# Optimization experiments

Measured on AMD Instinct MI355X. Metric: run time of the kernel, lower is better.

Reference implementation:

```python
import jax, jax.numpy as jnp
import numpy as np

EPS = 1e-5  # BatchNorm1d default eps
N1, N2 = 4096, 4096


def _encoder(x, W1, b1, W2, b2, W3, b3, gamma, beta):
    # fc1: Linear(node_num,256)+ReLU; fc2: Linear(256,128)+ReLU; fc3: Linear(128,64)+BN(train-mode)+ReLU
    h = jax.nn.relu(x @ W1.T + b1)
    h = jax.nn.relu(h @ W2.T + b2)
    h = h @ W3.T + b3
    m = h.mean(axis=0)
    v = ((h - m) ** 2).mean(axis=0)  # biased variance, as BN training mode
    return jax.nn.relu((h - m) / jnp.sqrt(v + EPS) * gamma + beta)


def _self_attention(x, adj, alpha):
    # vectorized form of the per-node double loop:
    # tmp_i = (sum_{j: adj[i,j]==1} alpha[i,j] * x[j]) / degree_i + x[i]  if degree_i != 0 else 0
    mask = (adj == 1.0).astype(x.dtype)           # [N,N]
    deg = adj.sum(axis=1, keepdims=True)          # [N,1]
    agg = (mask * alpha) @ x                      # [N,64] masked SpMM
    return jnp.where(deg != 0, agg / deg + x, jnp.zeros((), x.dtype))


def setup_inputs() -> dict:
    key = jax.random.key(0)
    ks = jax.random.split(key, 20)
    d = {}
    d["x1"] = jax.random.normal(ks[0], (N1, N1), jnp.float32)
    d["x2"] = jax.random.normal(ks[1], (N2, N2), jnp.float32)
    d["adj1"] = jax.random.bernoulli(ks[2], 0.01, (N1, N1)).astype(jnp.float32)
    d["adj2"] = jax.random.bernoulli(ks[3], 0.01, (N2, N2)).astype(jnp.float32)
    def lin(k, fan_out, fan_in):
        bound = 1.0 / np.sqrt(fan_in)
        k1, k2 = jax.random.split(k)
        return (jax.random.uniform(k1, (fan_out, fan_in), jnp.float32, -bound, bound),
                jax.random.uniform(k2, (fan_out,), jnp.float32, -bound, bound))
    d["e1_W1"], d["e1_b1"] = lin(ks[4], 256, N1)
    d["e1_W2"], d["e1_b2"] = lin(ks[5], 128, 256)
    d["e1_W3"], d["e1_b3"] = lin(ks[6], 64, 128)
    d["e1_gamma"] = jnp.ones((64,), jnp.float32)
    d["e1_beta"] = jnp.zeros((64,), jnp.float32)
    d["e2_W1"], d["e2_b1"] = lin(ks[7], 256, N2)
    d["e2_W2"], d["e2_b2"] = lin(ks[8], 128, 256)
    d["e2_W3"], d["e2_b3"] = lin(ks[9], 64, 128)
    d["e2_gamma"] = jnp.ones((64,), jnp.float32)
    d["e2_beta"] = jnp.zeros((64,), jnp.float32)
    d["alpha1"] = jax.random.uniform(ks[10], (N1, N1), jnp.float32)
    d["alpha2"] = jax.random.uniform(ks[11], (N2, N2), jnp.float32)
    d["Wc"], d["bc"] = lin(ks[12], 2, (N1 + N2) * 64)
    return d


def reference(x1, x2, adj1, adj2,
              e1_W1, e1_b1, e1_W2, e1_b2, e1_W3, e1_b3, e1_gamma, e1_beta,
              e2_W1, e2_b1, e2_W2, e2_b2, e2_W3, e2_b3, e2_gamma, e2_beta,
              alpha1, alpha2, Wc, bc):
    h1 = _encoder(x1, e1_W1, e1_b1, e1_W2, e1_b2, e1_W3, e1_b3, e1_gamma, e1_beta)
    h2 = _encoder(x2, e2_W1, e2_b1, e2_W2, e2_b2, e2_W3, e2_b3, e2_gamma, e2_beta)
    h1 = _self_attention(h1, adj1, alpha1)
    h2 = _self_attention(h2, adj2, alpha2)
    feat = jnp.concatenate([h1, h2], axis=0).reshape(1, -1)  # [1,(N1+N2)*64]
    return feat @ Wc.T + bc  # [1,2] logits (softmax is defined but unused in forward)
```

## Files before the change

kernel.cpp:

```cpp
#include <hip/hip_runtime.h>
#include <cstddef>
#include <cstdint>


#define NN 4096
#define HDIM 64
#define ENC_OUT (NN * HDIM)

typedef _Float16 half8 __attribute__((ext_vector_type(8)));
typedef _Float16 half4 __attribute__((ext_vector_type(4)));
typedef float v4f __attribute__((ext_vector_type(4)));

__device__ __forceinline__ void gld_lds16(const void* g, void* l) {
    __builtin_amdgcn_global_load_lds(
        (const __attribute__((address_space(1))) void*)g,
        (__attribute__((address_space(3))) void*)l, 16, 0, 0);
}

struct GemmP {
    const void*     A[2];
    const _Float16* B[2];
    const float*    bias[2];
    void*           C[2];
};

template<int NI, bool A16, int OUT, bool RELU>
__global__ __launch_bounds__(256) void gemm_kernel(GemmP p, int M, int lda, int Ksub)
{
    constexpr int N = NI * 64;
    __shared__ char Bs[NI * 4 * 1024];

    const int tid = threadIdx.x;
    const int wave = tid >> 6, lane = tid & 63;
    const int l16 = lane & 15, quad = lane >> 4;
    const int enc = blockIdx.z, split = blockIdx.x;
    const int m0 = blockIdx.y * 32;
    const int kOff = split * Ksub;
    const int nsteps = Ksub >> 5;

    const _Float16* __restrict__ Bp = p.B[enc];
    const char* Abase = (const char*)p.A[enc];

    const size_t aoff0 = (size_t)(m0 + l16) * lda + kOff + quad * 8;
    const size_t aoff1 = aoff0 + (size_t)16 * lda;

    half8 na0, na1;
    float4 nf0lo, nf0hi, nf1lo, nf1hi;
    auto loadA = [&](int s) {
        if constexpr (A16) {
            const _Float16* A = (const _Float16*)Abase;
            na0 = *(const half8*)(A + aoff0 + s * 32);
            na1 = *(const half8*)(A + aoff1 + s * 32);
        } else {
            const float* A = (const float*)Abase;
            nf0lo = *(const float4*)(A + aoff0 + s * 32);
            nf0hi = *(const float4*)(A + aoff0 + s * 32 + 4);
            nf1lo = *(const float4*)(A + aoff1 + s * 32);
            nf1hi = *(const float4*)(A + aoff1 + s * 32 + 4);
        }
    };

    v4f acc[2][NI];
#pragma unroll
    for (int mi = 0; mi < 2; mi++)
#pragma unroll
        for (int ni = 0; ni < NI; ni++) acc[mi][ni] = (v4f){0.f, 0.f, 0.f, 0.f};

    loadA(0);

    for (int s = 0; s < nsteps; ++s) {
#pragma unroll
        for (int ni = 0; ni < NI; ni++) {
            const int T = wave * NI + ni;
            const _Float16* g = Bp + (size_t)(T * 16 + l16) * lda + kOff + s * 32 + quad * 8;
            gld_lds16(g, &Bs[T * 1024]);
        }
        half8 ca0, ca1;
        if constexpr (A16) {
            ca0 = na0; ca1 = na1;
        } else {
            ca0[0] = (_Float16)nf0lo.x; ca0[1] = (_Float16)nf0lo.y;
            ca0[2] = (_Float16)nf0lo.z; ca0[3] = (_Float16)nf0lo.w;
            ca0[4] = (_Float16)nf0hi.x; ca0[5] = (_Float16)nf0hi.y;
            ca0[6] = (_Float16)nf0hi.z; ca0[7] = (_Float16)nf0hi.w;
            ca1[0] = (_Float16)nf1lo.x; ca1[1] = (_Float16)nf1lo.y;
            ca1[2] = (_Float16)nf1lo.z; ca1[3] = (_Float16)nf1lo.w;
            ca1[4] = (_Float16)nf1hi.x; ca1[5] = (_Float16)nf1hi.y;
            ca1[6] = (_Float16)nf1hi.z; ca1[7] = (_Float16)nf1hi.w;
        }
        if (s + 1 < nsteps) loadA(s + 1);

        __builtin_amdgcn_s_waitcnt(0x0F70);

#pragma unroll
        for (int ni = 0; ni < NI; ni++) {
            half8 bf = *(const half8*)&Bs[(wave * NI + ni) * 1024 + lane * 16];
            acc[0][ni] = __builtin_amdgcn_mfma_f32_16x16x32_f16(ca0, bf, acc[0][ni], 0, 0, 0);
            acc[1][ni] = __builtin_amdgcn_mfma_f32_16x16x32_f16(ca1, bf, acc[1][ni], 0, 0, 0);
        }
    }

#pragma unroll
    for (int mi = 0; mi < 2; mi++)
#pragma unroll
        for (int ni = 0; ni < NI; ni++) {
            const int col = wave * NI * 16 + ni * 16 + l16;
#pragma unroll
            for (int i = 0; i < 4; i++) {
                const int row = m0 + mi * 16 + quad * 4 + i;
                float v = acc[mi][ni][i];
                if constexpr (OUT == 2) {
                    ((_Float16*)p.C[0])[((size_t)(split * 2 + enc) * M + row) * N + col]
                        = (_Float16)v;
                } else {
                    v += p.bias[enc][col];
                    if (RELU) v = fmaxf(v, 0.f);
                    if constexpr (OUT == 0)
                        ((_Float16*)p.C[enc])[(size_t)row * N + col] = (_Float16)v;
                    else
                        ((float*)p.C[enc])[(size_t)row * N + col] = v;
                }
            }
        }
}

__global__ __launch_bounds__(256) void fc1_reduce_kernel(const _Float16* __restrict__ part,
                                                         const float* __restrict__ b0,
                                                         const float* __restrict__ b1,
                                                         _Float16* __restrict__ h1h)
{
    const size_t i = ((size_t)blockIdx.x * 256 + threadIdx.x) * 8;
    const int e = (int)(i >> 20);
    const size_t r = i & ((1u << 20) - 1);
    half8 p0 = *(const half8*)&part[((size_t)(0 * 2 + e) << 20) + r];
    half8 p1 = *(const half8*)&part[((size_t)(1 * 2 + e) << 20) + r];
    const int col = (int)(i & 255);
    const float* bs = e ? b1 : b0;
    float4 ba = *(const float4*)&bs[col];
    float4 bb = *(const float4*)&bs[col + 4];
    float b[8] = {ba.x, ba.y, ba.z, ba.w, bb.x, bb.y, bb.z, bb.w};
    half8 o;
#pragma unroll
    for (int j = 0; j < 8; j++) {
        float v = (float)p0[j] + (float)p1[j] + b[j];
        o[j] = (_Float16)fmaxf(v, 0.f);
    }
    *(half8*)&h1h[i] = o;
}

struct CvtJob { const float* s; _Float16* d; int n4; };
struct CvtP { CvtJob j[6]; };

__global__ __launch_bounds__(256) void cvt_all_kernel(CvtP p)
{
    int i = blockIdx.x * 256 + threadIdx.x;
#pragma unroll
    for (int k = 0; k < 6; k++) {
        if (i < p.j[k].n4) {
            float4 v = ((const float4*)p.j[k].s)[i];
            half4 h;
            h[0] = (_Float16)v.x; h[1] = (_Float16)v.y;
            h[2] = (_Float16)v.z; h[3] = (_Float16)v.w;
            ((half4*)p.j[k].d)[i] = h;
            return;
        }
        i -= p.j[k].n4;
    }
}

__global__ __launch_bounds__(256) void bn_stat1_kernel(const float* __restrict__ h3,
                                                       float* __restrict__ bnp)
{
    const int enc = blockIdx.y, b = blockIdx.x;
    const int c = threadIdx.x & 63, rg = threadIdx.x >> 6;
    const float* h = h3 + (size_t)enc * ENC_OUT + (size_t)b * 128 * HDIM;
    float s = 0.f, q = 0.f;
    for (int r = rg; r < 128; r += 4) {
        float v = h[(size_t)r * HDIM + c];
        s += v; q += v * v;
    }
    __shared__ float ss[4][64], sq[4][64];
    ss[rg][c] = s; sq[rg][c] = q;
    __syncthreads();
    if (threadIdx.x < 64) {
        float S = ss[0][c] + ss[1][c] + ss[2][c] + ss[3][c];
        float Q = sq[0][c] + sq[1][c] + sq[2][c] + sq[3][c];
        bnp[(size_t)(enc * 32 + b) * 128 + c] = S;
        bnp[(size_t)(enc * 32 + b) * 128 + 64 + c] = Q;
    }
}

__global__ void bn_stat2_kernel(const float* __restrict__ bnp, float* __restrict__ stats)
{
    const int enc = blockIdx.x, c = threadIdx.x;
    float s = 0.f, q = 0.f;
    for (int b = 0; b < 32; b++) {
        s += bnp[(size_t)(enc * 32 + b) * 128 + c];
        q += bnp[(size_t)(enc * 32 + b) * 128 + 64 + c];
    }
    float mean = s * (1.f / NN);
    float var = q * (1.f / NN) - mean * mean;
    stats[enc * 128 + c] = mean;
    stats[enc * 128 + 64 + c] = rsqrtf(var + 1e-5f);
}

__global__ __launch_bounds__(256) void bn_apply_kernel(const float* __restrict__ h3,
                                                       const float* __restrict__ stats,
                                                       const float* __restrict__ g0,
                                                       const float* __restrict__ g1,
                                                       const float* __restrict__ be0,
                                                       const float* __restrict__ be1,
                                                       float* __restrict__ hn)
{
    const int idx = blockIdx.x * 256 + threadIdx.x;
    const int enc = idx >> 18;
    const int c = idx & 63;
    const float* g = enc ? g1 : g0;
    const float* be = enc ? be1 : be0;
    const float m = stats[enc * 128 + c];
    const float rs = stats[enc * 128 + 64 + c];
    float v = (h3[idx] - m) * rs * g[c] + be[c];
    hn[idx] = fmaxf(v, 0.f);
}

__global__ __launch_bounds__(256) void att_kernel(const float* __restrict__ adj1,
                                                  const float* __restrict__ adj2,
                                                  const float* __restrict__ al1,
                                                  const float* __restrict__ al2,
                                                  const float* __restrict__ hn,
                                                  float* __restrict__ out)
{
    const int enc = blockIdx.y;
    const float* adj = enc ? adj2 : adj1;
    const float* al = enc ? al2 : al1;
    const float* h = hn + (size_t)enc * ENC_OUT;
    float* o = out + (size_t)enc * ENC_OUT;
    const int i = blockIdx.x;
    const int tid = threadIdx.x;

    __shared__ int s_cnt;
    __shared__ int s_j[128];
    __shared__ float s_w[128];
    __shared__ float s_acc[4][64];

    if (tid == 0) s_cnt = 0;
    __syncthreads();

    const float* arow = adj + (size_t)i * NN;
    const int jb = tid * 16;
#pragma unroll
    for (int q = 0; q < 4; q++) {
        float4 a = *(const float4*)&arow[jb + q * 4];
        if (a.x == 1.f) { int p = atomicAdd(&s_cnt, 1); if (p < 128) s_j[p] = jb + q * 4 + 0; }
        if (a.y == 1.f) { int p = atomicAdd(&s_cnt, 1); if (p < 128) s_j[p] = jb + q * 4 + 1; }
        if (a.z == 1.f) { int p = atomicAdd(&s_cnt, 1); if (p < 128) s_j[p] = jb + q * 4 + 2; }
        if (a.w == 1.f) { int p = atomicAdd(&s_cnt, 1); if (p < 128) s_j[p] = jb + q * 4 + 3; }
    }
    __syncthreads();
    const int cnt = min(s_cnt, 128);

    const float* alrow = al + (size_t)i * NN;
    for (int t = tid; t < cnt; t += 256) s_w[t] = alrow[s_j[t]];
    __syncthreads();

    const int c = tid & 63;
    const int g = tid >> 6;
    float acc = 0.f;
    for (int t = g; t < cnt; t += 4) acc += s_w[t] * h[(size_t)s_j[t] * HDIM + c];
    s_acc[g][c] = acc;
    __syncthreads();

    if (tid < 64) {
        float r;
        if (cnt != 0) {
            r = (s_acc[0][c] + s_acc[1][c] + s_acc[2][c] + s_acc[3][c]) / (float)cnt
                + h[(size_t)i * HDIM + c];
        } else {
            r = 0.f;
        }
        o[(size_t)i * HDIM + c] = r;
    }
}

#define FDIM (2 * ENC_OUT)

__global__ __launch_bounds__(256) void final_partial_kernel(const float* __restrict__ feat,
                                                            const float* __restrict__ Wc,
                                                            float* __restrict__ partial)
{
    const int gt = blockIdx.x * 256 + threadIdx.x;
    float p0 = 0.f, p1 = 0.f;
    for (int f = gt; f < FDIM; f += 131072) {
        float x = feat[f];
        p0 += x * Wc[f];
        p1 += x * Wc[FDIM + f];
    }
    __shared__ float r0[256], r1[256];
    r0[threadIdx.x] = p0;
    r1[threadIdx.x] = p1;
    __syncthreads();
    for (int off = 128; off > 0; off >>= 1) {
        if (threadIdx.x < off) {
            r0[threadIdx.x] += r0[threadIdx.x + off];
            r1[threadIdx.x] += r1[threadIdx.x + off];
        }
        __syncthreads();
    }
    if (threadIdx.x == 0) {
        partial[blockIdx.x * 2 + 0] = r0[0];
        partial[blockIdx.x * 2 + 1] = r1[0];
    }
}

__global__ void final_reduce_kernel(const float* __restrict__ partial,
                                    const float* __restrict__ bc,
                                    float* __restrict__ out)
{
    const int t = threadIdx.x;
    if (t < 2) {
        float s = bc[t];
        for (int b = 0; b < 512; b++) s += partial[b * 2 + t];
        out[t] = s;
    }
}


extern "C" void kernel_launch(void* const* d_in, const int* in_sizes, int n_in,
                              void* d_out, int out_size, void* d_ws, size_t ws_size,
                              hipStream_t stream)
{
    const float* x1    = (const float*)d_in[0];
    const float* x2    = (const float*)d_in[1];
    const float* adj1  = (const float*)d_in[2];
    const float* adj2  = (const float*)d_in[3];
    const float* e1_W1 = (const float*)d_in[4];
    const float* e1_b1 = (const float*)d_in[5];
    const float* e1_W2 = (const float*)d_in[6];
    const float* e1_b2 = (const float*)d_in[7];
    const float* e1_W3 = (const float*)d_in[8];
    const float* e1_b3 = (const float*)d_in[9];
    const float* e1_g  = (const float*)d_in[10];
    const float* e1_be = (const float*)d_in[11];
    const float* e2_W1 = (const float*)d_in[12];
    const float* e2_b1 = (const float*)d_in[13];
    const float* e2_W2 = (const float*)d_in[14];
    const float* e2_b2 = (const float*)d_in[15];
    const float* e2_W3 = (const float*)d_in[16];
    const float* e2_b3 = (const float*)d_in[17];
    const float* e2_g  = (const float*)d_in[18];
    const float* e2_be = (const float*)d_in[19];
    const float* alpha1 = (const float*)d_in[20];
    const float* alpha2 = (const float*)d_in[21];
    const float* Wc    = (const float*)d_in[22];
    const float* bc    = (const float*)d_in[23];
    (void)in_sizes; (void)n_in; (void)out_size; (void)ws_size;

    char* w = (char*)d_ws;
    _Float16* W1h = (_Float16*)w;  w += (size_t)2 * 256 * NN * 2;
    _Float16* W2h = (_Float16*)w;  w += (size_t)2 * 128 * 256 * 2;
    _Float16* W3h = (_Float16*)w;  w += (size_t)2 * 64 * 128 * 2;
    _Float16* h1h = (_Float16*)w;  w += (size_t)2 * NN * 256 * 2;
    char* shared8 = w;             w += (size_t)8 * 1024 * 1024;
    float* bnp = (float*)w;        w += (size_t)2 * 32 * 128 * 4;
    float* stats = (float*)w;      w += 256 * 4;
    float* hpart = (float*)w;      w += 1024 * 4;

    _Float16* part = (_Float16*)shared8;
    _Float16* h2h  = (_Float16*)shared8;
    float* h3  = (float*)(shared8 + 2 * 1024 * 1024);
    float* hn  = (float*)(shared8 + 4 * 1024 * 1024);
    float* att = (float*)(shared8 + 6 * 1024 * 1024);

    const dim3 blk(256);

    CvtP cp;
    cp.j[0] = { e1_W1, W1h,             262144 };
    cp.j[1] = { e2_W1, W1h + 256 * NN,  262144 };
    cp.j[2] = { e1_W2, W2h,             8192 };
    cp.j[3] = { e2_W2, W2h + 128 * 256, 8192 };
    cp.j[4] = { e1_W3, W3h,             2048 };
    cp.j[5] = { e2_W3, W3h + 64 * 128,  2048 };
    cvt_all_kernel<<<dim3(2128), blk, 0, stream>>>(cp);

    GemmP p1 = { {x1, x2}, {W1h, W1h + 256 * NN}, {e1_b1, e2_b1}, {part, part} };
    gemm_kernel<4, false, 2, false><<<dim3(2, NN / 32, 2), blk, 0, stream>>>(p1, NN, NN, 2048);
    fc1_reduce_kernel<<<dim3(1024), blk, 0, stream>>>(part, e1_b1, e2_b1, h1h);

    GemmP p2 = { {h1h, h1h + (size_t)NN * 256}, {W2h, W2h + 128 * 256}, {e1_b2, e2_b2},
                 {h2h, h2h + (size_t)NN * 128} };
    gemm_kernel<2, true, 0, true><<<dim3(1, NN / 32, 2), blk, 0, stream>>>(p2, NN, 256, 256);

    GemmP p3 = { {h2h, h2h + (size_t)NN * 128}, {W3h, W3h + 64 * 128}, {e1_b3, e2_b3},
                 {h3, h3 + ENC_OUT} };
    gemm_kernel<1, true, 1, false><<<dim3(1, NN / 32, 2), blk, 0, stream>>>(p3, NN, 128, 128);

    bn_stat1_kernel<<<dim3(32, 2), blk, 0, stream>>>(h3, bnp);
    bn_stat2_kernel<<<dim3(2), dim3(64), 0, stream>>>(bnp, stats);
    bn_apply_kernel<<<dim3(2 * ENC_OUT / 256), blk, 0, stream>>>(h3, stats, e1_g, e2_g,
                                                                 e1_be, e2_be, hn);

    att_kernel<<<dim3(NN, 2), blk, 0, stream>>>(adj1, adj2, alpha1, alpha2, hn, att);

    final_partial_kernel<<<dim3(512), blk, 0, stream>>>(att, Wc, hpart);
    final_reduce_kernel<<<dim3(1), dim3(64), 0, stream>>>(hpart, bc, (float*)d_out);
}
```

Before: 510.6 us.

## Fuse fc1 split-K into single 1024-thread kernel with in-LDS K reduction

Replaces the two-way split-K fc1 GEMM, its fp16 partial buffer and the separate reduce kernel with one kernel of 1024 threads per 32-row tile. Four wave groups each cover a quarter of K and are reduced through shared memory before bias and ReLU are applied. This removes the global round trip of the partials and one launch. In exchange each block uses 64KB of LDS and more barriers, and occupancy drops to 128 blocks per encoder with large blocks.

```diff
diff --git a/kernel.cpp b/kernel.cpp
--- a/kernel.cpp
+++ b/kernel.cpp
@@ -23,6 +23,125 @@
     const float*    bias[2];
     void*           C[2];
 };
+
+__global__ __launch_bounds__(1024) void fc1_kernel(GemmP p)
+{
+    __shared__ char Bs[64 * 1024];
+
+    const int tid = threadIdx.x;
+    const int wave = tid >> 6, lane = tid & 63;
+    const int l16 = lane & 15, quad = lane >> 4;
+    const int kg = wave >> 2, ng = wave & 3;
+    const int enc = blockIdx.y;
+    const int m0 = blockIdx.x * 32;
+    const int kOff = kg * 1024;
+    constexpr int nsteps = 1024 / 32;
+
+    const float* __restrict__ A = (const float*)p.A[enc];
+    const _Float16* __restrict__ Bb =
+        p.B[enc] + (size_t)(ng * 64 + l16) * NN + kOff + quad * 8;
+
+    const size_t aoff0 = (size_t)(m0 + l16) * NN + kOff + quad * 8;
+    const size_t aoff1 = aoff0 + (size_t)16 * NN;
+
+    float4 nf0lo, nf0hi, nf1lo, nf1hi;
+    auto loadA = [&](int s) {
+        nf0lo = *(const float4*)(A + aoff0 + s * 32);
+        nf0hi = *(const float4*)(A + aoff0 + s * 32 + 4);
+        nf1lo = *(const float4*)(A + aoff1 + s * 32);
+        nf1hi = *(const float4*)(A + aoff1 + s * 32 + 4);
+    };
+
+    v4f acc[2][4];
+#pragma unroll
+    for (int mi = 0; mi < 2; mi++)
+#pragma unroll
+        for (int ni = 0; ni < 4; ni++) acc[mi][ni] = (v4f){0.f, 0.f, 0.f, 0.f};
+
+    loadA(0);
+
+    for (int s = 0; s < nsteps; ++s) {
+#pragma unroll
+        for (int ni = 0; ni < 4; ni++)
+            gld_lds16(Bb + (size_t)ni * 16 * NN + s * 32, &Bs[(wave * 4 + ni) * 1024]);
+        __builtin_amdgcn_sched_barrier(0);
+
+        half8 ca0, ca1;
+        ca0[0] = (_Float16)nf0lo.x; ca0[1] = (_Float16)nf0lo.y;
+        ca0[2] = (_Float16)nf0lo.z; ca0[3] = (_Float16)nf0lo.w;
+        ca0[4] = (_Float16)nf0hi.x; ca0[5] = (_Float16)nf0hi.y;
+        ca0[6] = (_Float16)nf0hi.z; ca0[7] = (_Float16)nf0hi.w;
+        ca1[0] = (_Float16)nf1lo.x; ca1[1] = (_Float16)nf1lo.y;
+        ca1[2] = (_Float16)nf1lo.z; ca1[3] = (_Float16)nf1lo.w;
+        ca1[4] = (_Float16)nf1hi.x; ca1[5] = (_Float16)nf1hi.y;
+        ca1[6] = (_Float16)nf1hi.z; ca1[7] = (_Float16)nf1hi.w;
+
+        if (s + 1 < nsteps) {
+            loadA(s + 1);
+            __builtin_amdgcn_sched_barrier(0);
+            __builtin_amdgcn_s_waitcnt(0x0F74);
+        } else {
+            __builtin_amdgcn_sched_barrier(0);
+            __builtin_amdgcn_s_waitcnt(0x0F70);
+        }
+        __builtin_amdgcn_sched_barrier(0);
+
+#pragma unroll
+        for (int ni = 0; ni < 4; ni++) {
+            half8 bf = *(const half8*)&Bs[(wave * 4 + ni) * 1024 + lane * 16];
+            acc[0][ni] = __builtin_amdgcn_mfma_f32_16x16x32_f16(ca0, bf, acc[0][ni], 0, 0, 0);
+            acc[1][ni] = __builtin_amdgcn_mfma_f32_16x16x32_f16(ca1, bf, acc[1][ni], 0, 0, 0);
+        }
+    }
+
+    __syncthreads();
+
+    if (kg >= 2) {
+        const int sidx = (kg - 2) * 4 + ng;
+#pragma unroll
+        for (int mi = 0; mi < 2; mi++)
+#pragma unroll
+            for (int ni = 0; ni < 4; ni++)
+                *(v4f*)&Bs[sidx * 8192 + (mi * 4 + ni) * 1024 + lane * 16] = acc[mi][ni];
+    }
+    __syncthreads();
+    if (kg < 2) {
+        const int sidx = kg * 4 + ng;
+#pragma unroll
+        for (int mi = 0; mi < 2; mi++)
+#pragma unroll
+            for (int ni = 0; ni < 4; ni++)
+                acc[mi][ni] += *(const v4f*)&Bs[sidx * 8192 + (mi * 4 + ni) * 1024 + lane * 16];
+    }
+    __syncthreads();
+
+    if (kg == 1) {
+#pragma unroll
+        for (int mi = 0; mi < 2; mi++)
+#pragma unroll
+            for (int ni = 0; ni < 4; ni++)
+                *(v4f*)&Bs[ng * 8192 + (mi * 4 + ni) * 1024 + lane * 16] = acc[mi][ni];
+    }
+    __syncthreads();
+
+    if (kg == 0) {
+        _Float16* __restrict__ h1 = (_Float16*)p.C[enc];
+        const float* __restrict__ bs = p.bias[enc];
+#pragma unroll
+        for (int mi = 0; mi < 2; mi++)
+#pragma unroll
+            for (int ni = 0; ni < 4; ni++) {
+                v4f v = acc[mi][ni] + *(const v4f*)&Bs[ng * 8192 + (mi * 4 + ni) * 1024 + lane * 16];
+                const int col = ng * 64 + ni * 16 + l16;
+                const float b = bs[col];
+#pragma unroll
+                for (int i = 0; i < 4; i++) {
+                    const int row = m0 + mi * 16 + quad * 4 + i;
+                    h1[(size_t)row * 256 + col] = (_Float16)fmaxf(v[i] + b, 0.f);
+                }
+            }
+    }
+}
 
 template<int NI, bool A16, int OUT, bool RELU>
 __global__ __launch_bounds__(256) void gemm_kernel(GemmP p, int M, int lda, int Ksub)
@@ -109,43 +228,14 @@
             for (int i = 0; i < 4; i++) {
                 const int row = m0 + mi * 16 + quad * 4 + i;
                 float v = acc[mi][ni][i];
-                if constexpr (OUT == 2) {
-                    ((_Float16*)p.C[0])[((size_t)(split * 2 + enc) * M + row) * N + col]
-                        = (_Float16)v;
-                } else {
-                    v += p.bias[enc][col];
-                    if (RELU) v = fmaxf(v, 0.f);
-                    if constexpr (OUT == 0)
-                        ((_Float16*)p.C[enc])[(size_t)row * N + col] = (_Float16)v;
-                    else
-                        ((float*)p.C[enc])[(size_t)row * N + col] = v;
-                }
+                v += p.bias[enc][col];
+                if (RELU) v = fmaxf(v, 0.f);
+                if constexpr (OUT == 0)
+                    ((_Float16*)p.C[enc])[(size_t)row * N + col] = (_Float16)v;
+                else
+                    ((float*)p.C[enc])[(size_t)row * N + col] = v;
             }
         }
-}
-
-__global__ __launch_bounds__(256) void fc1_reduce_kernel(const _Float16* __restrict__ part,
-                                                         const float* __restrict__ b0,
-                                                         const float* __restrict__ b1,
-                                                         _Float16* __restrict__ h1h)
-{
-    const size_t i = ((size_t)blockIdx.x * 256 + threadIdx.x) * 8;
-    const int e = (int)(i >> 20);
-    const size_t r = i & ((1u << 20) - 1);
-    half8 p0 = *(const half8*)&part[((size_t)(0 * 2 + e) << 20) + r];
-    half8 p1 = *(const half8*)&part[((size_t)(1 * 2 + e) << 20) + r];
-    const int col = (int)(i & 255);
-    const float* bs = e ? b1 : b0;
-    float4 ba = *(const float4*)&bs[col];
-    float4 bb = *(const float4*)&bs[col + 4];
-    float b[8] = {ba.x, ba.y, ba.z, ba.w, bb.x, bb.y, bb.z, bb.w};
-    half8 o;
-#pragma unroll
-    for (int j = 0; j < 8; j++) {
-        float v = (float)p0[j] + (float)p1[j] + b[j];
-        o[j] = (_Float16)fmaxf(v, 0.f);
-    }
-    *(half8*)&h1h[i] = o;
 }
 
 struct CvtJob { const float* s; _Float16* d; int n4; };
@@ -365,7 +455,6 @@
     float* stats = (float*)w;      w += 256 * 4;
     float* hpart = (float*)w;      w += 1024 * 4;
 
-    _Float16* part = (_Float16*)shared8;
     _Float16* h2h  = (_Float16*)shared8;
     float* h3  = (float*)(shared8 + 2 * 1024 * 1024);
     float* hn  = (float*)(shared8 + 4 * 1024 * 1024);
@@ -382,9 +471,9 @@
     cp.j[5] = { e2_W3, W3h + 64 * 128,  2048 };
     cvt_all_kernel<<<dim3(2128), blk, 0, stream>>>(cp);
 
-    GemmP p1 = { {x1, x2}, {W1h, W1h + 256 * NN}, {e1_b1, e2_b1}, {part, part} };
-    gemm_kernel<4, false, 2, false><<<dim3(2, NN / 32, 2), blk, 0, stream>>>(p1, NN, NN, 2048);
-    fc1_reduce_kernel<<<dim3(1024), blk, 0, stream>>>(part, e1_b1, e2_b1, h1h);
+    GemmP p1 = { {x1, x2}, {W1h, W1h + 256 * NN}, {e1_b1, e2_b1},
+                 {h1h, h1h + (size_t)NN * 256} };
+    fc1_kernel<<<dim3(NN / 32, 2), dim3(1024), 0, stream>>>(p1);
 
     GemmP p2 = { {h1h, h1h + (size_t)NN * 256}, {W2h, W2h + 128 * 256}, {e1_b2, e2_b2},
                  {h2h, h2h + (size_t)NN * 128} };
```

Result: no change. 506.5 us (-0.8%).
